# Optimization experiments

Measured on AMD Instinct MI355X. Metric: run time of the kernel, lower is better.

Reference implementation:

```python
import jax, jax.numpy as jnp
import numpy as np

TIMELEN = 2016   # 288*7
T1 = 288         # steps per day
T3 = 864         # 288*3 time-graph nodes
LBAND = 3        # band width of time adjacency
N = 325          # input_dim = number of sensors
H = 325          # hidden_dim = num_nodes (conv channels)
B = 32
KSIZE = 577


def _norm_adj():
    # geneTimeAdj(864, L): banded time adjacency, symmetric, incl. self-loop
    i = np.arange(T3)
    A = (np.abs(i[:, None] - i[None, :]) <= LBAND).astype(np.float32)
    d = A.sum(1) ** -0.5
    return jnp.asarray(d[:, None] * A * d[None, :])  # D^-1/2 A D^-1/2


def setup_inputs() -> dict:
    key = jax.random.key(0)
    ks = jax.random.split(key, 12)

    def kaiming(k, fan_in, shape):
        bound = float(np.sqrt(6.0 / fan_in))
        return jax.random.uniform(k, shape, jnp.float32, -bound, bound)

    inp = {
        'input_feature': jax.random.normal(ks[0], (B, N, T1), jnp.float32),
        'x': jax.random.normal(ks[1], (TIMELEN, N), jnp.float32),  # standardized KB
        'w1': kaiming(ks[2], N, (N, H)), 'b1': jnp.zeros((H,), jnp.float32),
        'w11': kaiming(ks[3], H, (H, H)), 'b11': jnp.zeros((H,), jnp.float32),
        'w2': kaiming(ks[4], H, (H, H)), 'b2': jnp.zeros((H,), jnp.float32),
        'w22': kaiming(ks[5], H, (H, H)), 'b22': jnp.zeros((H,), jnp.float32),
        'w3': kaiming(ks[6], H, (H, H)), 'b3': jnp.zeros((H,), jnp.float32),
        'w33': kaiming(ks[7], H, (H, H)), 'b33': jnp.zeros((H,), jnp.float32),
        'conv_w': kaiming(ks[8], H * KSIZE, (H, H, KSIZE)),  # Conv1d(H->H, k=577)
        'conv_b': jnp.zeros((H,), jnp.float32),
        'week': jax.random.randint(ks[9], (B,), 0, 7, jnp.int32),
        'hour': jax.random.randint(ks[10], (B,), 0, T1, jnp.int32),
    }
    return inp


def reference(input_feature, x, w1, b1, w11, b11, w2, b2, w22, b22,
              w3, b3, w33, b33, conv_w, conv_b, week, hour):
    A = _norm_adj()
    c0 = jnp.concatenate([jnp.eye(T1, dtype=jnp.float32),
                          jnp.zeros((TIMELEN - T1, T1), jnp.float32)], 0)
    c10 = jnp.concatenate([jnp.eye(T3, dtype=jnp.float32),
                           jnp.zeros((TIMELEN - T3, T3), jnp.float32)], 0)
    shift = week * T1 + hour                      # per-sample circshift
    c = jax.vmap(lambda s: jnp.roll(c0, s, axis=0))(shift)        # [B,TL,288]
    c1 = jax.vmap(lambda s: jnp.roll(c10, s - T1, axis=0))(shift)  # [B,TL,864]

    cTx = jnp.einsum('btk,td->bkd', c, x)                          # [B,288,N]
    cin = jnp.einsum('btk,bkd->btd', c,
                     jnp.transpose(input_feature, (0, 2, 1)) - cTx)  # [B,TL,N]
    temp = jnp.einsum('btm,btd->bmd', c1, x + cin)                  # [B,864,N]

    def gcn(feat, w, b):
        support = jnp.einsum('bnd,do->bno', feat, w)
        return jnp.einsum('mn,bno->bmo', A, support) + b

    out = jnp.tanh(gcn(temp, w1, b1)) * jax.nn.sigmoid(gcn(temp, w11, b11))
    out = jnp.tanh(gcn(out, w2, b2)) * jax.nn.sigmoid(gcn(out, w22, b22))
    out = jnp.tanh(gcn(out, w3, b3)) * jax.nn.sigmoid(gcn(out, w33, b33))

    out = jnp.transpose(out, (0, 2, 1))  # [B,H,864]
    out = jax.lax.conv_general_dilated(
        out, conv_w, window_strides=(1,), padding='VALID',
        dimension_numbers=('NCH', 'OIH', 'NCH'))
    return out + conv_b[None, :, None]   # [B,H,288]
```

## Files before the change

kernel.cpp:

```cpp
#include <hip/hip_runtime.h>


typedef _Float16 half8 __attribute__((ext_vector_type(8)));
typedef float floatx4 __attribute__((ext_vector_type(4)));

#define DEV __device__ __forceinline__
#define AS1 __attribute__((address_space(1)))
#define AS3 __attribute__((address_space(3)))

constexpr int IPAD = 352;
constexpr int NPAD = 384;
constexpr int NFUSE = 768;
constexpr int MGCN = 32 * 864;
constexpr int MCONV = 32 * 288;
constexpr int KCONV_PAD = 203136;
constexpr int CONV_SPLITS = 7;
constexpr int CH32_TOTAL = KCONV_PAD / 32;
constexpr int CH32_PER = 907;

constexpr size_t OFF_XG = 0;
constexpr size_t SZ_XG_AL = 19465216;
constexpr size_t OFF_S = OFF_XG + SZ_XG_AL;
constexpr size_t SZ_S = (size_t)MGCN * NFUSE * 4;
constexpr size_t OFF_WG = OFF_S + SZ_S;
constexpr size_t SZ_WG = 6ull * NPAD * NPAD * 2;
constexpr size_t OFF_WCONV = OFF_WG + SZ_WG;
constexpr size_t OFF_CPART = OFF_S;

DEV void gload16(const void* g, void* l) {
    __builtin_amdgcn_global_load_lds((const AS1 void*)g, (AS3 void*)l, 16, 0, 0);
}

#define MEMFENCE() asm volatile("" ::: "memory")
#define BARRIER() do { MEMFENCE(); __builtin_amdgcn_s_barrier(); MEMFENCE(); } while (0)

__global__ void k_temp(const float* __restrict__ IF, const float* __restrict__ x,
                       const int* __restrict__ week, const int* __restrict__ hour,
                       _Float16* __restrict__ Xg) {
    int idx = blockIdx.x * 256 + threadIdx.x;
    if (idx >= MGCN * IPAD) return;
    int i  = idx % IPAD;
    int mm = idx / IPAD;
    int m  = mm % 864, b = mm / 864;
    float v = 0.f;
    if (i < 325) {
        if (m >= 288 && m < 576) {
            v = IF[((size_t)b * 325 + i) * 288 + (m - 288)];
        } else {
            int s  = week[b] * 288 + hour[b];
            int tm = (m + s + 1728) % 2016;
            v = x[(size_t)tm * 325 + i];
        }
    }
    Xg[(size_t)mm * IPAD + i] = (_Float16)v;
}

__global__ void k_pack_gcn(const float* w0, const float* w1, const float* w2,
                           const float* w3, const float* w4, const float* w5,
                           _Float16* __restrict__ Wg) {
    int idx = blockIdx.x * 256 + threadIdx.x;
    int d = idx % NPAD;
    int o = (idx / NPAD) % NPAD;
    int l = idx / (NPAD * NPAD);
    const float* w = l == 0 ? w0 : l == 1 ? w1 : l == 2 ? w2 : l == 3 ? w3 : l == 4 ? w4 : w5;
    float v = (o < 325 && d < 325) ? w[d * 325 + o] : 0.f;
    Wg[(size_t)idx] = (_Float16)v;
}

__global__ void k_pack_conv(const float* __restrict__ cw, _Float16* __restrict__ Wc) {
    __shared__ float tile[32][33];
    int o = blockIdx.x, i0 = blockIdx.y * 32, k0 = blockIdx.z * 32;
    int t = threadIdx.x;
    int c = t & 31, r4 = t >> 5;
#pragma unroll
    for (int p = 0; p < 4; ++p) {
        int ii = r4 * 4 + p;
        int i = i0 + ii, k = k0 + c;
        float v = 0.f;
        if (o < 325 && i < 325 && k < 577) v = cw[((size_t)o * 325 + i) * 577 + k];
        tile[ii][c] = v;
    }
    __syncthreads();
#pragma unroll
    for (int p = 0; p < 4; ++p) {
        int kk = r4 * 4 + p;
        int k = k0 + kk, i = i0 + c;
        int kidx = k * IPAD + i;
        if (kidx < KCONV_PAD) Wc[(size_t)o * KCONV_PAD + kidx] = (_Float16)tile[c][kk];
    }
}

__global__ __launch_bounds__(256) void k_gemm(const _Float16* __restrict__ Xg,
                                              const _Float16* __restrict__ Bw,
                                              float* __restrict__ C) {
    __shared__ _Float16 sA[128 * 64];
    __shared__ _Float16 sB[128 * 64];
    const int t = threadIdx.x;
    const int m0 = blockIdx.x * 128, n0 = blockIdx.y * 128;

    const int rj = t >> 3;
    const int cg = (t & 7) ^ (rj & 7);
    const _Float16* pa[4];
    const _Float16* pb[4];
#pragma unroll
    for (int j = 0; j < 4; ++j) {
        int m = m0 + j * 32 + rj;
        pa[j] = Xg + (size_t)m * IPAD + cg * 8;
        int n = n0 + j * 32 + rj;
        pb[j] = Bw + (size_t)n * NPAD + cg * 8;
    }

    const int lane = t & 63, wv = t >> 6;
    const int wm = wv >> 1, wn = wv & 1;
    const int r = lane & 15, q = lane >> 4, s8 = r & 7;
    int aRow[4], bRow[4];
#pragma unroll
    for (int i = 0; i < 4; ++i) {
        aRow[i] = (wm * 64 + i * 16 + r) * 64;
        bRow[i] = (wn * 64 + i * 16 + r) * 64;
    }
    const int xk0 = (q ^ s8) * 8;
    const int xk1 = ((q + 4) ^ s8) * 8;

    floatx4 acc[4][4] = {};

    for (int ch = 0; ch < 6; ++ch) {
        __syncthreads();
#pragma unroll
        for (int j = 0; j < 4; ++j) { gload16(pa[j], &sA[(j * 256 + t) * 8]); pa[j] += 64; }
#pragma unroll
        for (int j = 0; j < 4; ++j) { gload16(pb[j], &sB[(j * 256 + t) * 8]); pb[j] += 64; }
        __syncthreads();
#pragma unroll
        for (int kk = 0; kk < 2; ++kk) {
            const int xk = kk ? xk1 : xk0;
            half8 av[4], bv[4];
#pragma unroll
            for (int mi = 0; mi < 4; ++mi) av[mi] = *(const half8*)(sA + aRow[mi] + xk);
#pragma unroll
            for (int ni = 0; ni < 4; ++ni) bv[ni] = *(const half8*)(sB + bRow[ni] + xk);
#pragma unroll
            for (int mi = 0; mi < 4; ++mi)
#pragma unroll
                for (int ni = 0; ni < 4; ++ni)
                    acc[mi][ni] = __builtin_amdgcn_mfma_f32_16x16x32_f16(av[mi], bv[ni],
                                                                         acc[mi][ni], 0, 0, 0);
        }
    }

#pragma unroll
    for (int mi = 0; mi < 4; ++mi)
#pragma unroll
        for (int ni = 0; ni < 4; ++ni) {
            int row = m0 + wm * 64 + mi * 16 + q * 4;
            int col = n0 + wn * 64 + ni * 16 + r;
#pragma unroll
            for (int e = 0; e < 4; ++e)
                C[(size_t)(row + e) * NFUSE + col] = acc[mi][ni][e];
        }
}

__global__ __launch_bounds__(512, 2) void k_conv(const _Float16* __restrict__ Xg,
                                                 const _Float16* __restrict__ Wc,
                                                 float* __restrict__ C) {
    __shared__ _Float16 lds[3 * 20480];
    const int t = threadIdx.x;
    const int m0 = blockIdx.x * 256;
    const int chunk0 = blockIdx.y * CH32_PER;
    int nch = CH32_TOTAL - chunk0;
    if (nch > CH32_PER) nch = CH32_PER;

    const _Float16* src[5];
    int ldsoff[5];
#pragma unroll
    for (int p = 0; p < 2; ++p) {
        int s = t + p * 512;
        int j = s >> 3, cc = s & 7;
        int g = cc ^ (j & 7);
        int m = m0 + 2 * j + (g >> 2);
        int mrow = m + (m / 288) * 576;
        src[p] = Xg + (size_t)mrow * IPAD + (size_t)chunk0 * 32 + (g & 3) * 8;
        ldsoff[p] = s * 16;
    }
#pragma unroll
    for (int p = 0; p < 3; ++p) {
        int s = t + p * 512;
        int j = s >> 3, cc = s & 7;
        int g = cc ^ (j & 7);
        int n = 2 * j + (g >> 2);
        src[2 + p] = Wc + (size_t)n * KCONV_PAD + (size_t)chunk0 * 32 + (g & 3) * 8;
        ldsoff[2 + p] = 16384 + s * 16;
    }

    const int lane = t & 63, wv = t >> 6;
    const int wm = wv >> 1, wn = wv & 1;
    const int r = lane & 15, q = lane >> 4;
    int row_a = wm * 64 + r;
    int aoff0 = (row_a >> 1) * 128 + ((((row_a & 1) << 2) | q) ^ ((row_a >> 1) & 7)) * 16;
    int row_b = wn * 192 + r;
    int boff0 = 16384 + (row_b >> 1) * 128 +
                ((((row_b & 1) << 2) | q) ^ ((row_b >> 1) & 7)) * 16;

    floatx4 acc[4][12] = {};

    auto stage = [&](int lc, int buf) {
        char* dst = (char*)lds + buf * 40960;
        size_t adv = (size_t)lc * 32;
#pragma unroll
        for (int p = 0; p < 5; ++p)
            gload16(src[p] + adv, dst + ldsoff[p]);
    };

    stage(0, 0);
    stage(1, 1);

    int buf = 0;
    for (int lc = 0; lc < nch; ++lc) {
        int pre = lc + 2;  if (pre > nch - 1) pre = nch - 1;
        int pbuf = buf + 2; if (pbuf >= 3) pbuf -= 3;
        stage(pre, pbuf);
        asm volatile("s_waitcnt vmcnt(10)" ::: "memory");
        BARRIER();
        const char* cb = (const char*)lds + buf * 40960;
        half8 av[4];
#pragma unroll
        for (int mi = 0; mi < 4; ++mi)
            av[mi] = *(const half8*)(cb + aoff0 + mi * 1024);
#pragma unroll
        for (int ni = 0; ni < 12; ++ni) {
            half8 bv = *(const half8*)(cb + boff0 + ni * 1024);
#pragma unroll
            for (int mi = 0; mi < 4; ++mi)
                acc[mi][ni] = __builtin_amdgcn_mfma_f32_16x16x32_f16(av[mi], bv,
                                                                     acc[mi][ni], 0, 0, 0);
        }
        BARRIER();
        buf = (buf + 1 == 3) ? 0 : buf + 1;
    }
    asm volatile("s_waitcnt vmcnt(0)" ::: "memory");

#pragma unroll
    for (int mi = 0; mi < 4; ++mi)
#pragma unroll
        for (int ni = 0; ni < 12; ++ni) {
            int row = m0 + wm * 64 + mi * 16 + q * 4;
            int col = wn * 192 + ni * 16 + r;
#pragma unroll
            for (int e = 0; e < 4; ++e)
                unsafeAtomicAdd(&C[(size_t)(row + e) * NPAD + col], acc[mi][ni][e]);
        }
}

__global__ void k_bandact(const float* __restrict__ S,
                          const float* __restrict__ b1, const float* __restrict__ b2,
                          _Float16* __restrict__ Xg) {
    int bm = blockIdx.x;
    int m = bm % 864;
    int dm = (m < 3 ? m : 3) + ((863 - m) < 3 ? (863 - m) : 3) + 1;
    for (int o = threadIdx.x; o < 325; o += 256) {
        float g1 = b1[o], g2 = b2[o];
#pragma unroll
        for (int dn = -3; dn <= 3; ++dn) {
            int n = m + dn;
            if (n < 0 || n > 863) continue;
            int dnd = (n < 3 ? n : 3) + ((863 - n) < 3 ? (863 - n) : 3) + 1;
            float a = rsqrtf((float)(dm * dnd));
            size_t off = (size_t)(bm + dn) * NFUSE + o;
            g1 += a * S[off];
            g2 += a * S[off + NPAD];
        }
        float vt = tanhf(g1);
        float vs = 1.f / (1.f + expf(-g2));
        Xg[(size_t)bm * IPAD + o] = (_Float16)(vt * vs);
    }
}

__global__ void k_reduce(const float* __restrict__ Cp, const float* __restrict__ cb,
                         float* __restrict__ out) {
    __shared__ float tile[32][33];
    int b = blockIdx.x, t0 = blockIdx.y * 32, o0 = blockIdx.z * 32;
    int t = threadIdx.x;
    int c = t & 31, r4 = t >> 5;
#pragma unroll
    for (int p = 0; p < 4; ++p) {
        int tt = r4 * 4 + p;
        tile[tt][c] = Cp[(size_t)(b * 288 + t0 + tt) * NPAD + (o0 + c)];
    }
    __syncthreads();
#pragma unroll
    for (int p = 0; p < 4; ++p) {
        int oo = r4 * 4 + p;
        int o = o0 + oo;
        if (o < 325)
            out[((size_t)b * 325 + o) * 288 + t0 + c] = tile[c][oo] + cb[o];
    }
}

extern "C" void kernel_launch(void* const* d_in, const int* in_sizes, int n_in,
                              void* d_out, int out_size, void* d_ws, size_t ws_size,
                              hipStream_t stream) {
    const float* IF = (const float*)d_in[0];
    const float* x  = (const float*)d_in[1];
    const float* wg[6] = {(const float*)d_in[2],  (const float*)d_in[4],
                          (const float*)d_in[6],  (const float*)d_in[8],
                          (const float*)d_in[10], (const float*)d_in[12]};
    const float* bg[6] = {(const float*)d_in[3],  (const float*)d_in[5],
                          (const float*)d_in[7],  (const float*)d_in[9],
                          (const float*)d_in[11], (const float*)d_in[13]};
    const float* cw  = (const float*)d_in[14];
    const float* cb  = (const float*)d_in[15];
    const int* week  = (const int*)d_in[16];
    const int* hour  = (const int*)d_in[17];
    float* out = (float*)d_out;

    char* ws = (char*)d_ws;
    _Float16* Xg = (_Float16*)(ws + OFF_XG);
    float* S     = (float*)(ws + OFF_S);
    _Float16* Wg = (_Float16*)(ws + OFF_WG);
    _Float16* Wc = (_Float16*)(ws + OFF_WCONV);
    float* Cp    = (float*)(ws + OFF_CPART);

    k_pack_gcn<<<(6 * NPAD * NPAD) / 256, 256, 0, stream>>>(wg[0], wg[1], wg[2], wg[3],
                                                            wg[4], wg[5], Wg);
    k_pack_conv<<<dim3(NPAD, 11, 19), 256, 0, stream>>>(cw, Wc);
    k_temp<<<(MGCN * IPAD) / 256, 256, 0, stream>>>(IF, x, week, hour, Xg);

    for (int l = 0; l < 3; ++l) {
        k_gemm<<<dim3(MGCN / 128, NFUSE / 128), 256, 0, stream>>>(
            Xg, Wg + (size_t)(2 * l) * NPAD * NPAD, S);
        k_bandact<<<MGCN, 256, 0, stream>>>(S, bg[2 * l], bg[2 * l + 1], Xg);
    }

    hipMemsetAsync(Cp, 0, (size_t)MCONV * NPAD * 4, stream);
    k_conv<<<dim3(MCONV / 256, CONV_SPLITS), 512, 0, stream>>>(Xg, Wc, Cp);

    k_reduce<<<dim3(32, 9, 11), 256, 0, stream>>>(Cp, cb, out);
}
```

Baseline: 2.041 ms.

## Reshape conv GEMM warp tiling and interleave LDS reads with prioritized MFMA phases

Changes the conv GEMM wave layout from a 4x2 grid (64x192 per wave) to a 2x4 grid (128x96 per wave). B fragments are loaded once per chunk and A fragments in four pairs. Each pair is followed by a block barrier, an lgkm wait, a sched_barrier and raised wave priority around its MFMA burst. The intent is a ping-pong style schedule where some waves issue MFMAs while others do LDS reads, at the cost of extra barriers per chunk.

```diff
diff --git a/kernel.cpp b/kernel.cpp
--- a/kernel.cpp
+++ b/kernel.cpp
@@ -193,15 +193,15 @@
     }
 
     const int lane = t & 63, wv = t >> 6;
-    const int wm = wv >> 1, wn = wv & 1;
+    const int wm = wv >> 2, wn = wv & 3;
     const int r = lane & 15, q = lane >> 4;
-    int row_a = wm * 64 + r;
+    int row_a = wm * 128 + r;
     int aoff0 = (row_a >> 1) * 128 + ((((row_a & 1) << 2) | q) ^ ((row_a >> 1) & 7)) * 16;
-    int row_b = wn * 192 + r;
+    int row_b = wn * 96 + r;
     int boff0 = 16384 + (row_b >> 1) * 128 +
                 ((((row_b & 1) << 2) | q) ^ ((row_b >> 1) & 7)) * 16;
 
-    floatx4 acc[4][12] = {};
+    floatx4 acc[8][6] = {};
 
     auto stage = [&](int lc, int buf) {
         char* dst = (char*)lds + buf * 40960;
@@ -222,29 +222,53 @@
         asm volatile("s_waitcnt vmcnt(10)" ::: "memory");
         BARRIER();
         const char* cb = (const char*)lds + buf * 40960;
-        half8 av[4];
-#pragma unroll
-        for (int mi = 0; mi < 4; ++mi)
-            av[mi] = *(const half8*)(cb + aoff0 + mi * 1024);
-#pragma unroll
-        for (int ni = 0; ni < 12; ++ni) {
-            half8 bv = *(const half8*)(cb + boff0 + ni * 1024);
-#pragma unroll
-            for (int mi = 0; mi < 4; ++mi)
-                acc[mi][ni] = __builtin_amdgcn_mfma_f32_16x16x32_f16(av[mi], bv,
-                                                                     acc[mi][ni], 0, 0, 0);
-        }
+
+        half8 bv[6];
+#pragma unroll
+        for (int ni = 0; ni < 6; ++ni)
+            bv[ni] = *(const half8*)(cb + boff0 + ni * 1024);
+        half8 av0 = *(const half8*)(cb + aoff0);
+        half8 av1 = *(const half8*)(cb + aoff0 + 1024);
+        BARRIER();
+        asm volatile("s_waitcnt lgkmcnt(0)" ::: "memory");
+        __builtin_amdgcn_sched_barrier(0);
+        __builtin_amdgcn_s_setprio(1);
+#pragma unroll
+        for (int ni = 0; ni < 6; ++ni) {
+            acc[0][ni] = __builtin_amdgcn_mfma_f32_16x16x32_f16(av0, bv[ni], acc[0][ni], 0, 0, 0);
+            acc[1][ni] = __builtin_amdgcn_mfma_f32_16x16x32_f16(av1, bv[ni], acc[1][ni], 0, 0, 0);
+        }
+        __builtin_amdgcn_s_setprio(0);
+
+#pragma unroll
+        for (int p = 1; p < 4; ++p) {
+            half8 a0 = *(const half8*)(cb + aoff0 + (2 * p) * 1024);
+            half8 a1 = *(const half8*)(cb + aoff0 + (2 * p + 1) * 1024);
+            BARRIER();
+            asm volatile("s_waitcnt lgkmcnt(0)" ::: "memory");
+            __builtin_amdgcn_sched_barrier(0);
+            __builtin_amdgcn_s_setprio(1);
+#pragma unroll
+            for (int ni = 0; ni < 6; ++ni) {
+                acc[2 * p][ni] =
+                    __builtin_amdgcn_mfma_f32_16x16x32_f16(a0, bv[ni], acc[2 * p][ni], 0, 0, 0);
+                acc[2 * p + 1][ni] =
+                    __builtin_amdgcn_mfma_f32_16x16x32_f16(a1, bv[ni], acc[2 * p + 1][ni], 0, 0, 0);
+            }
+            __builtin_amdgcn_s_setprio(0);
+        }
+
         BARRIER();
         buf = (buf + 1 == 3) ? 0 : buf + 1;
     }
     asm volatile("s_waitcnt vmcnt(0)" ::: "memory");
 
 #pragma unroll
-    for (int mi = 0; mi < 4; ++mi)
-#pragma unroll
-        for (int ni = 0; ni < 12; ++ni) {
-            int row = m0 + wm * 64 + mi * 16 + q * 4;
-            int col = wn * 192 + ni * 16 + r;
+    for (int mi = 0; mi < 8; ++mi)
+#pragma unroll
+        for (int ni = 0; ni < 6; ++ni) {
+            int row = m0 + wm * 128 + mi * 16 + q * 4;
+            int col = wn * 96 + ni * 16 + r;
 #pragma unroll
             for (int e = 0; e < 4; ++e)
                 unsafeAtomicAdd(&C[(size_t)(row + e) * NPAD + col], acc[mi][ni][e]);
```

Result: slower. 2.084 ms (+2.1%).
